# Optimization experiments

Hardware: AMD Instinct MI355X
Metric: run time of the kernel (lower is better)

The kernel has to match this reference:

```python
import jax, jax.numpy as jnp
import numpy as np
from jax.scipy.linalg import expm

B, S, D, E, K, NROT = 2, 2048, 1024, 8, 2, 3
EPS = 1e-5


def setup_inputs() -> dict:
    key = jax.random.key(0)
    ks = jax.random.split(key, 16)
    sc = 0.02
    x = jax.random.normal(ks[0], (B, S, D), jnp.float32)
    ln_gamma = 1.0 + sc * jax.random.normal(ks[1], (D,), jnp.float32)
    ln_beta = sc * jax.random.normal(ks[2], (D,), jnp.float32)
    abel_w = sc * jax.random.normal(ks[3], (D, D), jnp.float32)
    abel_b = sc * jax.random.normal(ks[4], (D,), jnp.float32)
    moe_gate_w = sc * jax.random.normal(ks[5], (D, E), jnp.float32)
    moe_gate_b = sc * jax.random.normal(ks[6], (E,), jnp.float32)
    ew1 = sc * jax.random.normal(ks[7], (E, D, 2 * D), jnp.float32)
    eb1 = sc * jax.random.normal(ks[8], (E, 2 * D), jnp.float32)
    ew2 = sc * jax.random.normal(ks[9], (E, 2 * D, D), jnp.float32)
    eb2 = sc * jax.random.normal(ks[10], (E, D), jnp.float32)
    g = sc * jax.random.normal(ks[11], (NROT, D, D), jnp.float32)
    gens = 0.5 * (g - jnp.swapaxes(g, -1, -2))  # skew-symmetric, as in reset_parameters
    gc_w = sc * jax.random.normal(ks[12], (2 * D, 1), jnp.float32)
    gc_b = sc * jax.random.normal(ks[13], (1,), jnp.float32)
    return dict(x=x, ln_gamma=ln_gamma, ln_beta=ln_beta, abel_w=abel_w, abel_b=abel_b,
                moe_gate_w=moe_gate_w, moe_gate_b=moe_gate_b, ew1=ew1, eb1=eb1,
                ew2=ew2, eb2=eb2, gens=gens, gc_w=gc_w, gc_b=gc_b)


def _gelu(x):
    return jax.nn.gelu(x, approximate=False)  # torch nn.GELU default = exact erf


def _forward(x, ln_gamma, ln_beta, abel_w, abel_b, moe_gate_w, moe_gate_b,
             ew1, eb1, ew2, eb2, gens, gc_w, gc_b):
    residual = x
    # LayerNorm
    mu = jnp.mean(x, axis=-1, keepdims=True)
    var = jnp.mean((x - mu) ** 2, axis=-1, keepdims=True)
    xn = (x - mu) * jax.lax.rsqrt(var + EPS) * ln_gamma + ln_beta
    # abel branch: Linear + GELU
    abel_out = _gelu(xn @ abel_w + abel_b)
    # MoE: dense all-experts compute, masked by top-k softmax weights
    logits = xn @ moe_gate_w + moe_gate_b                      # [B,S,E]
    topw, topi = jax.lax.top_k(logits, K)                      # [B,S,K]
    topw = jax.nn.softmax(topw, axis=-1)
    w_dense = jnp.sum(jax.nn.one_hot(topi, E, dtype=xn.dtype) * topw[..., None], axis=-2)  # [B,S,E]
    h = _gelu(jnp.einsum('bsd,edh->ebsh', xn, ew1) + eb1[:, None, None, :])  # [E,B,S,2D]
    eo = jnp.einsum('ebsh,ehd->ebsd', h, ew2) + eb2[:, None, None, :]        # [E,B,S,D]
    moe_out = jnp.einsum('ebsd,bse->bsd', eo, w_dense)
    # GeometricRotation: sequential matrix_exp rotations
    for i in range(NROT):
        moe_out = moe_out @ expm(gens[i])
    # gated residual mix
    combined = jnp.concatenate([abel_out, moe_out], axis=-1)
    gate = jax.nn.sigmoid(combined @ gc_w + gc_b)              # [B,S,1]
    mixed = abel_out * (1.0 - gate) + moe_out * gate
    return residual + mixed


def reference(x, ln_gamma, ln_beta, abel_w, abel_b, moe_gate_w, moe_gate_b,
              ew1, eb1, ew2, eb2, gens, gc_w, gc_b):
    return _forward(x, ln_gamma, ln_beta, abel_w, abel_b, moe_gate_w, moe_gate_b,
                    ew1, eb1, ew2, eb2, gens, gc_w, gc_b)
```

## Files before the change

kernel.cpp:

```cpp
#include <hip/hip_runtime.h>
#include <hip/hip_bf16.h>
#include <cstdint>
#include <cstddef>

#define DD   1024
#define DD2  2048
#define EE   8
#define NTOK 4096
#define CAPR 9216
#define MAXT 72

typedef __bf16 bf16_t;
typedef __bf16 bf16x8 __attribute__((ext_vector_type(8)));
typedef __bf16 bf16x4 __attribute__((ext_vector_type(4)));
typedef float  f32x4v __attribute__((ext_vector_type(4)));

__device__ __forceinline__ float gelu_f(float v){
  const float t = v*(0.7978845608028654f + 0.0356774081f*v*v);
  const float u = __expf(2.0f*t);
  return __fdividef(v*u, 1.0f + u);
}

__device__ __forceinline__ void gload_lds16(const void* g, void* l){
  __builtin_amdgcn_global_load_lds(
    (const __attribute__((address_space(1))) unsigned int*)(uintptr_t)g,
    (__attribute__((address_space(3))) unsigned int*)(uintptr_t)l,
    16, 0, 0);
}

enum { EPI_GELU_F32=0, EPI_GELU_BF16=1, EPI_BIAS_BF16=2, EPI_SCALE_BF16=3,
       EPI_ADDV_BF16=4, EPI_BF16=5, EPI_F32=6 };

template<int BM,int BN,int EPI,bool TAB>
__global__ __launch_bounds__(256)
void gemm_bt(const bf16_t* __restrict__ A, const bf16_t* __restrict__ Bt,
             const int N, const int K, const int gx, const int gy, const int gz,
             const long sAz, const long sBz, const long sOz,
             const int* __restrict__ tileE, const int* __restrict__ tileR,
             const int* __restrict__ ntp, const int* __restrict__ offp,
             const int* __restrict__ tokOf,
             const float* __restrict__ bias, const long sBias,
             const float alpha,
             const bf16_t* __restrict__ addv,
             float* __restrict__ outF, bf16_t* __restrict__ outB)
{
  constexpr int BK = 32;
  constexpr int WM = BM/2, WN = BN/2;
  constexpr int FM = WM/16, FN = WN/16;
  constexpr int IA = BM/64, IB = BN/64;
  constexpr int NLD = IA + IB;
  __shared__ alignas(16) bf16_t sA[3][BM*BK];
  __shared__ alignas(16) bf16_t sB[3][BN*BK];

  int bx, by, bz; long ro = 0;
  if constexpr (TAB) {
    const int nwg = gx * gy;
    const int q = nwg >> 3, r = nwg & 7;
    const int k = blockIdx.x & 7, i = blockIdx.x >> 3;
    if (i >= q + (k < r ? 1 : 0)) return;
    const int l = k * q + (k < r ? k : r) + i;
    const int ti = l / gx; bx = l - ti*gx;
    if (ti >= ntp[0]) return;
    bz = tileE[ti]; by = 0;
    ro = (long)offp[bz] + tileR[ti];
  } else {
    const int nwg = gx * gy * gz;
    const int q = nwg >> 3, r = nwg & 7;
    const int k = blockIdx.x & 7, i = blockIdx.x >> 3;
    if (i >= q + (k < r ? 1 : 0)) return;
    const int l = k * q + (k < r ? k : r) + i;
    bx = l % gx; const int t2 = l / gx; by = t2 % gy; bz = t2 / gy;
  }

  const int z = bz;
  const bf16_t* Bp = Bt + (size_t)z * sBz;
  float*  oF = outF;
  bf16_t* oB = outB;
  if constexpr (TAB) {
    oB += ro * (long)N;
  } else {
    A += (size_t)z * sAz;
    if (oF) oF += (size_t)z * sOz;
    if (oB) oB += (size_t)z * sOz;
  }
  const float*  bp = bias ? bias + (size_t)z * sBias : nullptr;
  const bf16_t* vp = addv ? addv + (size_t)z * sOz   : nullptr;

  const int tid = threadIdx.x;
  const int wid = tid >> 6, lid = tid & 63;
  const int wr = wid >> 1, wc = wid & 1;
  const int brow = by * BM, bcol = bx * BN;
  const int fr = lid & 15, fq = lid >> 4;
  const int rl = lid >> 2, qs = lid & 3;

  const char* aSrc[IA];
  const char* bSrc[IB];
  #pragma unroll
  for (int i = 0; i < IA; i++) {
    const int rloc = (wid*IA + i)*16 + rl;
    const int q = qs ^ ((rloc >> 1) & 3);
    const bf16_t* arow;
    if constexpr (TAB) {
      arow = tokOf ? (A + (size_t)tokOf[ro + rloc] * K)
                   : (A + (size_t)(ro + rloc) * K);
    } else {
      arow = A + (size_t)(brow + rloc) * K;
    }
    aSrc[i] = (const char*)arow + q*16;
  }
  #pragma unroll
  for (int i = 0; i < IB; i++) {
    const int rloc = (wid*IB + i)*16 + rl;
    const int q = qs ^ ((rloc >> 1) & 3);
    bSrc[i] = (const char*)(Bp + (size_t)(bcol + rloc) * K) + q*16;
  }

  f32x4v acc[FM][FN] = {};

  auto stage = [&](int buf, int kt) {
    #pragma unroll
    for (int i = 0; i < IA; i++)
      gload_lds16(aSrc[i] + (size_t)kt*2, (char*)sA[buf] + (wid*IA + i)*1024);
    #pragma unroll
    for (int i = 0; i < IB; i++)
      gload_lds16(bSrc[i] + (size_t)kt*2, (char*)sB[buf] + (wid*IB + i)*1024);
  };

  stage(0, 0);
  stage(1, BK);
  const int nk = K / BK;
  int b0 = 0, b1 = 1, b2 = 2;

  for (int t = 0; t < nk; ++t) {
    if (t < nk - 1) asm volatile("s_waitcnt vmcnt(%0)" :: "i"(NLD) : "memory");
    else            asm volatile("s_waitcnt vmcnt(0)" ::: "memory");
    __builtin_amdgcn_s_barrier();
    __builtin_amdgcn_sched_barrier(0);
    if (t + 2 < nk) stage(b2, (t + 2)*BK);

    bf16x8 af[FM], bb[FN];
    #pragma unroll
    for (int mi = 0; mi < FM; mi++) {
      const int r2 = wr*WM + mi*16 + fr;
      const int q = fq ^ ((r2 >> 1) & 3);
      af[mi] = *(const bf16x8*)((const char*)sA[b0] + r2*64 + q*16);
    }
    #pragma unroll
    for (int ni = 0; ni < FN; ni++) {
      const int r2 = wc*WN + ni*16 + fr;
      const int q = fq ^ ((r2 >> 1) & 3);
      bb[ni] = *(const bf16x8*)((const char*)sB[b0] + r2*64 + q*16);
    }
    #pragma unroll
    for (int mi = 0; mi < FM; mi++)
      #pragma unroll
      for (int ni = 0; ni < FN; ni++)
        acc[mi][ni] = __builtin_amdgcn_mfma_f32_16x16x32_bf16(
            af[mi], bb[ni], acc[mi][ni], 0, 0, 0);

    const int tb_ = b0; b0 = b1; b1 = b2; b2 = tb_;
  }

  #pragma unroll
  for (int mi = 0; mi < FM; mi++) {
    #pragma unroll
    for (int ni = 0; ni < FN; ni++) {
      const int rg0 = brow + wr*WM + mi*16 + fq*4;
      const int cg  = bcol + wc*WN + ni*16 + fr;
      #pragma unroll
      for (int i = 0; i < 4; i++) {
        const int rg = rg0 + i;
        float v = acc[mi][ni][i];
        if constexpr (EPI == EPI_GELU_F32) {
          v += bp[cg];
          oF[(size_t)rg*N + cg] = gelu_f(v);
        } else if constexpr (EPI == EPI_GELU_BF16) {
          v += bp[cg];
          oB[(size_t)rg*N + cg] = (bf16_t)gelu_f(v);
        } else if constexpr (EPI == EPI_BIAS_BF16) {
          v += bp[cg];
          oB[(size_t)rg*N + cg] = (bf16_t)v;
        } else if constexpr (EPI == EPI_SCALE_BF16) {
          oB[(size_t)rg*N + cg] = (bf16_t)(v * alpha);
        } else if constexpr (EPI == EPI_ADDV_BF16) {
          oB[(size_t)rg*N + cg] = (bf16_t)(v + (float)vp[(size_t)rg*N + cg]);
        } else if constexpr (EPI == EPI_BF16) {
          oB[(size_t)rg*N + cg] = (bf16_t)v;
        } else {
          oF[(size_t)rg*N + cg] = v;
        }
      }
    }
  }
}

__device__ __forceinline__ void tcvt_tile(const float* __restrict__ src,
                                          bf16_t* __restrict__ dst,
                                          int R, int C, int bx, int by,
                                          float (*t)[65]){
  const int c0 = bx*64, r0 = by*64;
  const int lx = threadIdx.x & 15, ly = threadIdx.x >> 4;
  #pragma unroll
  for (int i = 0; i < 4; i++) {
    const int row = r0 + ly + i*16;
    const float4 v = *(const float4*)(src + (size_t)row*C + c0 + lx*4);
    t[ly + i*16][lx*4+0] = v.x; t[ly + i*16][lx*4+1] = v.y;
    t[ly + i*16][lx*4+2] = v.z; t[ly + i*16][lx*4+3] = v.w;
  }
  __syncthreads();
  #pragma unroll
  for (int i = 0; i < 4; i++) {
    const int c = c0 + ly + i*16;
    bf16x4 o;
    #pragma unroll
    for (int j = 0; j < 4; j++) o[j] = (bf16_t)t[lx*4+j][ly + i*16];
    *(bf16x4*)(dst + (size_t)c*R + r0 + lx*4) = o;
  }
}

__global__ __launch_bounds__(256)
void prep_kernel(const float* __restrict__ abel_w, bf16_t* __restrict__ abel_wT,
                 const float* __restrict__ ew1, bf16_t* __restrict__ ew1T,
                 const float* __restrict__ ew2, bf16_t* __restrict__ ew2T,
                 const float* __restrict__ gens, bf16_t* __restrict__ Hn)
{
  __shared__ float t[64][65];
  const int bid = blockIdx.x;
  if (bid < 256) {
    tcvt_tile(abel_w, abel_wT, DD, DD, bid & 15, bid >> 4, t);
  } else if (bid < 4352) {
    const int i = bid - 256, z = i >> 9, r = i & 511;
    tcvt_tile(ew1 + (size_t)z*DD*DD2, ew1T + (size_t)z*DD2*DD, DD, DD2, r & 31, r >> 5, t);
  } else if (bid < 8448) {
    const int i = bid - 4352, z = i >> 9, r = i & 511;
    tcvt_tile(ew2 + (size_t)z*DD2*DD, ew2T + (size_t)z*DD*DD2, DD2, DD, r & 15, r >> 4, t);
  } else {
    const long i4 = ((long)(bid - 8448)*256 + threadIdx.x)*4;
    const float4 v = *(const float4*)(gens + i4);
    bf16x4 b; b[0]=(bf16_t)(-v.x); b[1]=(bf16_t)(-v.y);
    b[2]=(bf16_t)(-v.z); b[3]=(bf16_t)(-v.w);
    *(bf16x4*)(Hn + i4) = b;
  }
}

__global__ __launch_bounds__(256)
void tb16_kernel(const bf16_t* __restrict__ Ut, bf16_t* __restrict__ Tb){
  __shared__ bf16_t tile[32][33];
  const bf16_t* src = Ut + (size_t)(1 - blockIdx.z) * DD * DD;
  bf16_t*       dst = Tb + (size_t)blockIdx.z * DD * DD;
  const int c0 = blockIdx.x*32, r0 = blockIdx.y*32;
  #pragma unroll
  for (int i = 0; i < 4; i++)
    tile[threadIdx.y + i*8][threadIdx.x] = src[(size_t)(r0 + threadIdx.y + i*8)*DD + c0 + threadIdx.x];
  __syncthreads();
  #pragma unroll
  for (int i = 0; i < 4; i++)
    dst[(size_t)(c0 + threadIdx.y + i*8)*DD + r0 + threadIdx.x] = tile[threadIdx.x][threadIdx.y + i*8];
}

__global__ __launch_bounds__(256)
void vw_kernel(const bf16_t* __restrict__ Hn, const bf16_t* __restrict__ H2,
               bf16_t* __restrict__ Vb, bf16_t* __restrict__ Wtb){
  const long i0 = ((long)blockIdx.x*256 + threadIdx.x)*4;
  const long rc = i0 % (long)(DD*DD);
  const int r = (int)(rc / DD), c0 = (int)(rc % DD);
  const bf16x4 h  = *(const bf16x4*)(Hn + i0);
  const bf16x4 h2 = *(const bf16x4*)(H2 + i0);
  bf16x4 v, w;
  #pragma unroll
  for (int j = 0; j < 4; j++) {
    const float d  = (r == c0 + j) ? 1.0f : 0.0f;
    const float fh = (float)h[j], f2 = (float)h2[j];
    v[j] = (bf16_t)(d + fh + f2*0.5f);
    w[j] = (bf16_t)(d*(1.0f/6.0f) - fh*(1.0f/24.0f) + f2*(1.0f/120.0f));
  }
  *(bf16x4*)(Vb  + i0) = v;
  *(bf16x4*)(Wtb + i0) = w;
}

__global__ __launch_bounds__(256)
void ln_gate_kernel(const float* __restrict__ x, const float* __restrict__ gamma,
                    const float* __restrict__ beta, const float* __restrict__ gw,
                    const float* __restrict__ gb,
                    bf16_t* __restrict__ xnb, int2* __restrict__ ids,
                    float2* __restrict__ wts)
{
  const int t = blockIdx.x, tid = threadIdx.x, j0 = tid*4;
  const int wid = tid >> 6, lid = tid & 63;
  const float4 v = *(const float4*)(x + (size_t)t*DD + j0);
  float s  = v.x + v.y + v.z + v.w;
  float ss = v.x*v.x + v.y*v.y + v.z*v.z + v.w*v.w;
  #pragma unroll
  for (int off = 32; off; off >>= 1) { s += __shfl_down(s, off); ss += __shfl_down(ss, off); }
  __shared__ float redS[4], redQ[4], mv[2];
  if (lid == 0) { redS[wid] = s; redQ[wid] = ss; }
  __syncthreads();
  if (tid == 0) {
    const float S1 = redS[0]+redS[1]+redS[2]+redS[3];
    const float S2 = redQ[0]+redQ[1]+redQ[2]+redQ[3];
    const float mu  = S1 * (1.0f/DD);
    const float var = S2 * (1.0f/DD) - mu*mu;
    mv[0] = mu; mv[1] = rsqrtf(var + 1e-5f);
  }
  __syncthreads();
  const float mu = mv[0], rstd = mv[1];
  const float4 g = *(const float4*)(gamma + j0);
  const float4 b = *(const float4*)(beta  + j0);
  float xn[4];
  xn[0] = (v.x-mu)*rstd*g.x + b.x;
  xn[1] = (v.y-mu)*rstd*g.y + b.y;
  xn[2] = (v.z-mu)*rstd*g.z + b.z;
  xn[3] = (v.w-mu)*rstd*g.w + b.w;
  bf16x4 ov; ov[0]=(bf16_t)xn[0]; ov[1]=(bf16_t)xn[1]; ov[2]=(bf16_t)xn[2]; ov[3]=(bf16_t)xn[3];
  *(bf16x4*)(xnb + (size_t)t*DD + j0) = ov;

  float p[8] = {0,0,0,0,0,0,0,0};
  #pragma unroll
  for (int i = 0; i < 4; i++) {
    const float4 a0 = *(const float4*)(gw + (size_t)(j0+i)*EE);
    const float4 a1 = *(const float4*)(gw + (size_t)(j0+i)*EE + 4);
    const float xv = xn[i];
    p[0]+=xv*a0.x; p[1]+=xv*a0.y; p[2]+=xv*a0.z; p[3]+=xv*a0.w;
    p[4]+=xv*a1.x; p[5]+=xv*a1.y; p[6]+=xv*a1.z; p[7]+=xv*a1.w;
  }
  #pragma unroll
  for (int off = 32; off; off >>= 1) {
    #pragma unroll
    for (int e = 0; e < 8; e++) p[e] += __shfl_down(p[e], off);
  }
  __shared__ float pr[32];
  if (lid == 0) {
    #pragma unroll
    for (int e = 0; e < 8; e++) pr[wid*8 + e] = p[e];
  }
  __syncthreads();
  if (tid == 0) {
    float l[8];
    #pragma unroll
    for (int e = 0; e < 8; e++) l[e] = pr[e] + pr[8+e] + pr[16+e] + pr[24+e] + gb[e];
    int i1 = 0; float m1 = l[0];
    #pragma unroll
    for (int e = 1; e < 8; e++) if (l[e] > m1) { m1 = l[e]; i1 = e; }
    int i2 = 0; float m2 = -1e30f;
    #pragma unroll
    for (int e = 0; e < 8; e++) if (e != i1 && l[e] > m2) { m2 = l[e]; i2 = e; }
    const float wa = 1.0f/(1.0f + expf(m2 - m1));
    ids[t] = make_int2(i1, i2);
    wts[t] = make_float2(wa, 1.0f - wa);
  }
}

__global__ __launch_bounds__(256)
void route_kernel(const int2* __restrict__ ids, int* __restrict__ slotA,
                  int* __restrict__ slotB, int* __restrict__ cnt,
                  int* __restrict__ off, int* __restrict__ tileE,
                  int* __restrict__ tileR, int* __restrict__ ntp)
{
  const int tid = threadIdx.x;
  const int wid = tid >> 6, lid = tid & 63;
  __shared__ int wsum[EE][4];
  __shared__ int base[EE];
  if (tid < EE) base[tid] = 0;
  __syncthreads();
  const unsigned long long lt = (1ull << lid) - 1ull;
  for (int c0 = 0; c0 < NTOK; c0 += 256) {
    const int t = c0 + tid;
    const int2 id = ids[t];
    int pA = 0, pB = 0;
    #pragma unroll
    for (int e = 0; e < EE; e++) {
      const bool fA = (id.x == e), fB = (id.y == e);
      const unsigned long long mA = __ballot(fA);
      const unsigned long long mB = __ballot(fB);
      const int cA = __popcll(mA);
      if (lid == 0) wsum[e][wid] = cA + __popcll(mB);
      if (fA) pA = __popcll(mA & lt);
      if (fB) pB = cA + __popcll(mB & lt);
    }
    __syncthreads();
    int wbA = base[id.x], wbB = base[id.y];
    for (int w = 0; w < wid; w++) { wbA += wsum[id.x][w]; wbB += wsum[id.y][w]; }
    slotA[t] = wbA + pA;
    slotB[t] = wbB + pB;
    __syncthreads();
    if (tid < EE) base[tid] += wsum[tid][0]+wsum[tid][1]+wsum[tid][2]+wsum[tid][3];
    __syncthreads();
  }
  if (tid == 0) {
    int a = 0, nt = 0;
    for (int e = 0; e < EE; e++) {
      cnt[e] = base[e]; off[e] = a;
      for (int r2 = 0; r2 < base[e]; r2 += 128) { tileE[nt] = e; tileR[nt] = r2; nt++; }
      a += (base[e] + 127) & ~127;
    }
    ntp[0] = nt;
  }
}

__global__ __launch_bounds__(256)
void fill_tok_kernel(const int2* __restrict__ ids, const int* __restrict__ slotA,
                     const int* __restrict__ slotB, const int* __restrict__ off,
                     const int* __restrict__ cnt, int* __restrict__ tokOf){
  const int t = blockIdx.x*256 + threadIdx.x;
  const int2 id = ids[t];
  tokOf[off[id.x] + slotA[t]] = t;
  tokOf[off[id.y] + slotB[t]] = t;
  if (blockIdx.x == 0) {
    for (int e = 0; e < EE; e++) {
      const int c = cnt[e], o = off[e], al = (c + 127) & ~127;
      for (int p = c + threadIdx.x; p < al; p += 256) tokOf[o + p] = 0;
    }
  }
}

__global__ __launch_bounds__(256)
void combine_kernel(const bf16_t* __restrict__ Yg, const int2* __restrict__ ids,
                    const int* __restrict__ slotA, const int* __restrict__ slotB,
                    const int* __restrict__ off, const float2* __restrict__ wts,
                    bf16_t* __restrict__ Xa){
  const int t = blockIdx.x, j = threadIdx.x*4;
  const int2 id = ids[t];
  const float2 w = wts[t];
  const bf16x4 a = *(const bf16x4*)(Yg + (size_t)(off[id.x] + slotA[t])*DD + j);
  const bf16x4 b = *(const bf16x4*)(Yg + (size_t)(off[id.y] + slotB[t])*DD + j);
  bf16x4 o;
  #pragma unroll
  for (int i = 0; i < 4; i++) o[i] = (bf16_t)(w.x*(float)a[i] + w.y*(float)b[i]);
  *(bf16x4*)(Xa + (size_t)t*DD + j) = o;
}

__global__ __launch_bounds__(256)
void mix_kernel(const float* __restrict__ x, const bf16_t* __restrict__ abel,
                const float* __restrict__ rot, const float* __restrict__ gcw,
                const float* __restrict__ gcb, float* __restrict__ out)
{
  const int t = blockIdx.x, tid = threadIdx.x, j0 = tid*4;
  const int wid = tid >> 6, lid = tid & 63;
  const bf16x4 ab = *(const bf16x4*)(abel + (size_t)t*DD + j0);
  const float4 r  = *(const float4*)(rot  + (size_t)t*DD + j0);
  const float4 ga = *(const float4*)(gcw + j0);
  const float4 gr = *(const float4*)(gcw + DD + j0);
  const float a0 = (float)ab[0], a1 = (float)ab[1], a2 = (float)ab[2], a3 = (float)ab[3];
  float p = a0*ga.x + a1*ga.y + a2*ga.z + a3*ga.w
          + r.x*gr.x + r.y*gr.y + r.z*gr.z + r.w*gr.w;
  #pragma unroll
  for (int off = 32; off; off >>= 1) p += __shfl_down(p, off);
  __shared__ float red[4];
  __shared__ float gsh;
  if (lid == 0) red[wid] = p;
  __syncthreads();
  if (tid == 0) {
    const float P = red[0] + red[1] + red[2] + red[3] + gcb[0];
    gsh = 1.0f/(1.0f + expf(-P));
  }
  __syncthreads();
  const float gate = gsh, g1 = 1.0f - gate;
  const float4 xv = *(const float4*)(x + (size_t)t*DD + j0);
  float4 o;
  o.x = xv.x + a0*g1 + r.x*gate;
  o.y = xv.y + a1*g1 + r.y*gate;
  o.z = xv.z + a2*g1 + r.z*gate;
  o.w = xv.w + a3*g1 + r.w*gate;
  *(float4*)(out + (size_t)t*DD + j0) = o;
}

extern "C" void kernel_launch(void* const* d_in, const int* in_sizes, int n_in,
                              void* d_out, int out_size, void* d_ws, size_t ws_size,
                              hipStream_t stream)
{
  (void)in_sizes; (void)n_in; (void)out_size; (void)ws_size;
  const float* x      = (const float*)d_in[0];
  const float* ln_g   = (const float*)d_in[1];
  const float* ln_b   = (const float*)d_in[2];
  const float* abel_w = (const float*)d_in[3];
  const float* abel_b = (const float*)d_in[4];
  const float* gate_w = (const float*)d_in[5];
  const float* gate_b = (const float*)d_in[6];
  const float* ew1    = (const float*)d_in[7];
  const float* eb1    = (const float*)d_in[8];
  const float* ew2    = (const float*)d_in[9];
  const float* eb2    = (const float*)d_in[10];
  const float* gens   = (const float*)d_in[11];
  const float* gc_w   = (const float*)d_in[12];
  const float* gc_b   = (const float*)d_in[13];
  float* out = (float*)d_out;

  char* wsp = (char*)d_ws;
  auto alloc = [&](size_t bytes) -> char* {
    char* p = wsp; wsp += (bytes + 255) & ~(size_t)255; return p;
  };
  const size_t MB = 1u<<20;
  bf16_t* xnb   = (bf16_t*)alloc((size_t)NTOK*DD*2);
  int2*   ids   = (int2*)  alloc((size_t)NTOK*8);
  float2* wts   = (float2*)alloc((size_t)NTOK*8);
  int*    slotA = (int*)   alloc((size_t)NTOK*4);
  int*    slotB = (int*)   alloc((size_t)NTOK*4);
  int*    cnt   = (int*)   alloc(64);
  int*    off   = (int*)   alloc(64);
  int*    tileE = (int*)   alloc(MAXT*4);
  int*    tileR = (int*)   alloc(MAXT*4);
  int*    ntp   = (int*)   alloc(64);
  int*    tokOf = (int*)   alloc((size_t)CAPR*4);
  bf16_t* abel_wT = (bf16_t*)alloc((size_t)DD*DD*2);
  char*   UN      = alloc(64*MB);
  bf16_t* ew1T  = (bf16_t*)UN;
  bf16_t* ew2T  = (bf16_t*)(UN + 32*MB);
  bf16_t* Hn    = (bf16_t*)alloc((size_t)3*DD*DD*2);
  bf16_t* abelo = (bf16_t*)alloc((size_t)NTOK*DD*2);
  bf16_t* Yg    = (bf16_t*)alloc((size_t)CAPR*DD*2);
  bf16_t* Hg    = (bf16_t*)alloc((size_t)CAPR*DD2*2);
  bf16_t* Xa    = (bf16_t*)alloc((size_t)NTOK*DD*2);
  float*  rot   = (float*)Hg;
  bf16_t* H2  = (bf16_t*)(UN + 0*MB);
  bf16_t* H3  = (bf16_t*)(UN + 6*MB);
  bf16_t* Vb  = (bf16_t*)(UN + 12*MB);
  bf16_t* Wtb = (bf16_t*)(UN + 18*MB);
  bf16_t* Ut  = (bf16_t*)(UN + 24*MB);
  bf16_t* Tb  = (bf16_t*)(UN + 30*MB);
  bf16_t* Pb  = (bf16_t*)(UN + 34*MB);
  bf16_t* Rt  = (bf16_t*)(UN + 36*MB);
  const long D2 = (long)DD*DD;

  auto gflat = [](int gx, int gy, int gz) {
    const int nwg = gx*gy*gz; return 8 * ((nwg + 7) / 8);
  };

  prep_kernel<<<dim3(11520,1,1), 256, 0, stream>>>(abel_w, abel_wT, ew1, ew1T,
                                                   ew2, ew2T, gens, Hn);

  ln_gate_kernel<<<dim3(NTOK,1,1), 256, 0, stream>>>(x, ln_g, ln_b, gate_w, gate_b,
                                                     xnb, ids, wts);
  route_kernel<<<dim3(1,1,1), 256, 0, stream>>>(ids, slotA, slotB, cnt, off,
                                                tileE, tileR, ntp);
  fill_tok_kernel<<<dim3(NTOK/256,1,1), 256, 0, stream>>>(ids, slotA, slotB, off, cnt, tokOf);

  gemm_bt<128,128,EPI_GELU_BF16,true><<<dim3((DD2/128)*MAXT,1,1), 256, 0, stream>>>(
      xnb, ew1T, DD2, DD, DD2/128, MAXT, 1, 0, (long)DD2*DD, 0,
      tileE, tileR, ntp, off, tokOf, eb1, DD2, 1.0f, nullptr, nullptr, Hg);
  gemm_bt<128,128,EPI_BIAS_BF16,true><<<dim3((DD/128)*MAXT,1,1), 256, 0, stream>>>(
      Hg, ew2T, DD, DD2, DD/128, MAXT, 1, 0, (long)DD*DD2, 0,
      tileE, tileR, ntp, off, nullptr, eb2, DD, 1.0f, nullptr, nullptr, Yg);
  combine_kernel<<<dim3(NTOK,1,1), 256, 0, stream>>>(Yg, ids, slotA, slotB, off, wts, Xa);

  gemm_bt<128,128,EPI_GELU_BF16,false><<<dim3(gflat(8,32,1),1,1), 256, 0, stream>>>(
      xnb, abel_wT, DD, DD, 8, 32, 1, 0, 0, 0, nullptr, nullptr, nullptr, nullptr,
      nullptr, abel_b, 0, 1.0f, nullptr, nullptr, abelo);

  gemm_bt<64,64,EPI_SCALE_BF16,false><<<dim3(gflat(16,16,3),1,1), 256, 0, stream>>>(
      Hn, Hn, DD, DD, 16, 16, 3, D2, D2, D2, nullptr, nullptr, nullptr, nullptr,
      nullptr, nullptr, 0, -1.0f, nullptr, nullptr, H2);
  gemm_bt<64,64,EPI_SCALE_BF16,false><<<dim3(gflat(16,16,3),1,1), 256, 0, stream>>>(
      H2, Hn, DD, DD, 16, 16, 3, D2, D2, D2, nullptr, nullptr, nullptr, nullptr,
      nullptr, nullptr, 0, -1.0f, nullptr, nullptr, H3);
  vw_kernel<<<dim3(3*DD*DD/1024,1,1), 256, 0, stream>>>(Hn, H2, Vb, Wtb);
  gemm_bt<64,64,EPI_ADDV_BF16,false><<<dim3(gflat(16,16,3),1,1), 256, 0, stream>>>(
      H3, Wtb, DD, DD, 16, 16, 3, D2, D2, D2, nullptr, nullptr, nullptr, nullptr,
      nullptr, nullptr, 0, 1.0f, Vb, nullptr, Ut);
  tb16_kernel<<<dim3(32,32,2), dim3(32,8,1), 0, stream>>>(Ut, Tb);
  gemm_bt<64,64,EPI_BF16,false><<<dim3(gflat(16,16,1),1,1), 256, 0, stream>>>(
      Ut + 2*D2, Tb, DD, DD, 16, 16, 1, 0, 0, 0, nullptr, nullptr, nullptr, nullptr,
      nullptr, nullptr, 0, 1.0f, nullptr, nullptr, Pb);
  gemm_bt<64,64,EPI_BF16,false><<<dim3(gflat(16,16,1),1,1), 256, 0, stream>>>(
      Pb, Tb + D2, DD, DD, 16, 16, 1, 0, 0, 0, nullptr, nullptr, nullptr, nullptr,
      nullptr, nullptr, 0, 1.0f, nullptr, nullptr, Rt);
  gemm_bt<128,128,EPI_F32,false><<<dim3(gflat(8,32,1),1,1), 256, 0, stream>>>(
      Xa, Rt, DD, DD, 8, 32, 1, 0, 0, 0, nullptr, nullptr, nullptr, nullptr,
      nullptr, nullptr, 0, 1.0f, nullptr, rot, nullptr);

  mix_kernel<<<dim3(NTOK,1,1), 256, 0, stream>>>(x, abelo, rot, gc_w, gc_b, out);
}
```

Baseline: 329.1 us.

## Use 256-row 8-wave tiles for expert GEMM1 and batch prep transposes

```diff
diff --git a/kernel.cpp b/kernel.cpp
--- a/kernel.cpp
+++ b/kernel.cpp
@@ -7,8 +7,9 @@
 #define DD2  2048
 #define EE   8
 #define NTOK 4096
-#define CAPR 9216
-#define MAXT 72
+#define CAPR 10240
+#define MAXT1 72
+#define MAXT2 40
 
 typedef __bf16 bf16_t;
 typedef __bf16 bf16x8 __attribute__((ext_vector_type(8)));
@@ -31,8 +32,8 @@
 enum { EPI_GELU_F32=0, EPI_GELU_BF16=1, EPI_BIAS_BF16=2, EPI_SCALE_BF16=3,
        EPI_ADDV_BF16=4, EPI_BF16=5, EPI_F32=6 };
 
-template<int BM,int BN,int EPI,bool TAB>
-__global__ __launch_bounds__(256)
+template<int BM,int BN,int WAVES,int EPI,bool TAB>
+__global__ __launch_bounds__(WAVES*64)
 void gemm_bt(const bf16_t* __restrict__ A, const bf16_t* __restrict__ Bt,
              const int N, const int K, const int gx, const int gy, const int gz,
              const long sAz, const long sBz, const long sOz,
@@ -45,9 +46,10 @@
              float* __restrict__ outF, bf16_t* __restrict__ outB)
 {
   constexpr int BK = 32;
-  constexpr int WM = BM/2, WN = BN/2;
+  constexpr int WROWS = WAVES/2;
+  constexpr int WM = BM/WROWS, WN = BN/2;
   constexpr int FM = WM/16, FN = WN/16;
-  constexpr int IA = BM/64, IB = BN/64;
+  constexpr int IA = BM/(16*WAVES), IB = BN/(16*WAVES);
   constexpr int NLD = IA + IB;
   __shared__ alignas(16) bf16_t sA[3][BM*BK];
   __shared__ alignas(16) bf16_t sB[3][BN*BK];
@@ -194,28 +196,25 @@
   }
 }
 
-__device__ __forceinline__ void tcvt_tile(const float* __restrict__ src,
-                                          bf16_t* __restrict__ dst,
-                                          int R, int C, int bx, int by,
-                                          float (*t)[65]){
-  const int c0 = bx*64, r0 = by*64;
-  const int lx = threadIdx.x & 15, ly = threadIdx.x >> 4;
-  #pragma unroll
-  for (int i = 0; i < 4; i++) {
-    const int row = r0 + ly + i*16;
-    const float4 v = *(const float4*)(src + (size_t)row*C + c0 + lx*4);
-    t[ly + i*16][lx*4+0] = v.x; t[ly + i*16][lx*4+1] = v.y;
-    t[ly + i*16][lx*4+2] = v.z; t[ly + i*16][lx*4+3] = v.w;
-  }
-  __syncthreads();
-  #pragma unroll
-  for (int i = 0; i < 4; i++) {
-    const int c = c0 + ly + i*16;
-    bf16x4 o;
-    #pragma unroll
-    for (int j = 0; j < 4; j++) o[j] = (bf16_t)t[lx*4+j][ly + i*16];
-    *(bf16x4*)(dst + (size_t)c*R + r0 + lx*4) = o;
-  }
+struct TileRef { const float* src; bf16_t* dst; int R, C, bx, by; };
+
+__device__ __forceinline__ TileRef resolve_tile(
+    int ti, const float* abel_w, bf16_t* abel_wT,
+    const float* ew1, bf16_t* ew1T, const float* ew2, bf16_t* ew2T){
+  TileRef tr;
+  if (ti < 256) {
+    tr.src = abel_w; tr.dst = abel_wT; tr.R = DD; tr.C = DD;
+    tr.bx = ti & 15; tr.by = ti >> 4;
+  } else if (ti < 4352) {
+    const int i = ti - 256, z = i >> 9, r = i & 511;
+    tr.src = ew1 + (size_t)z*DD*DD2; tr.dst = ew1T + (size_t)z*DD2*DD;
+    tr.R = DD; tr.C = DD2; tr.bx = r & 31; tr.by = r >> 5;
+  } else {
+    const int i = ti - 4352, z = i >> 9, r = i & 511;
+    tr.src = ew2 + (size_t)z*DD2*DD; tr.dst = ew2T + (size_t)z*DD*DD2;
+    tr.R = DD2; tr.C = DD; tr.bx = r & 15; tr.by = r >> 4;
+  }
+  return tr;
 }
 
 __global__ __launch_bounds__(256)
@@ -224,22 +223,57 @@
                  const float* __restrict__ ew2, bf16_t* __restrict__ ew2T,
                  const float* __restrict__ gens, bf16_t* __restrict__ Hn)
 {
-  __shared__ float t[64][65];
   const int bid = blockIdx.x;
-  if (bid < 256) {
-    tcvt_tile(abel_w, abel_wT, DD, DD, bid & 15, bid >> 4, t);
-  } else if (bid < 4352) {
-    const int i = bid - 256, z = i >> 9, r = i & 511;
-    tcvt_tile(ew1 + (size_t)z*DD*DD2, ew1T + (size_t)z*DD2*DD, DD, DD2, r & 31, r >> 5, t);
-  } else if (bid < 8448) {
-    const int i = bid - 4352, z = i >> 9, r = i & 511;
-    tcvt_tile(ew2 + (size_t)z*DD2*DD, ew2T + (size_t)z*DD*DD2, DD2, DD, r & 15, r >> 4, t);
+  const int lx = threadIdx.x & 15, ly = threadIdx.x >> 4;
+  if (bid < 4224) {
+    __shared__ float t[64][65];
+    const TileRef t0 = resolve_tile(bid*2,     abel_w, abel_wT, ew1, ew1T, ew2, ew2T);
+    const TileRef t1 = resolve_tile(bid*2 + 1, abel_w, abel_wT, ew1, ew1T, ew2, ew2T);
+    float4 g0[4], g1[4];
+    #pragma unroll
+    for (int i = 0; i < 4; i++)
+      g0[i] = *(const float4*)(t0.src + (size_t)(t0.by*64 + ly + i*16)*t0.C + t0.bx*64 + lx*4);
+    #pragma unroll
+    for (int i = 0; i < 4; i++)
+      g1[i] = *(const float4*)(t1.src + (size_t)(t1.by*64 + ly + i*16)*t1.C + t1.bx*64 + lx*4);
+    #pragma unroll
+    for (int i = 0; i < 4; i++) {
+      t[ly + i*16][lx*4+0] = g0[i].x; t[ly + i*16][lx*4+1] = g0[i].y;
+      t[ly + i*16][lx*4+2] = g0[i].z; t[ly + i*16][lx*4+3] = g0[i].w;
+    }
+    __syncthreads();
+    #pragma unroll
+    for (int i = 0; i < 4; i++) {
+      const int c = t0.bx*64 + ly + i*16;
+      bf16x4 o;
+      #pragma unroll
+      for (int j = 0; j < 4; j++) o[j] = (bf16_t)t[lx*4+j][ly + i*16];
+      *(bf16x4*)(t0.dst + (size_t)c*t0.R + t0.by*64 + lx*4) = o;
+    }
+    __syncthreads();
+    #pragma unroll
+    for (int i = 0; i < 4; i++) {
+      t[ly + i*16][lx*4+0] = g1[i].x; t[ly + i*16][lx*4+1] = g1[i].y;
+      t[ly + i*16][lx*4+2] = g1[i].z; t[ly + i*16][lx*4+3] = g1[i].w;
+    }
+    __syncthreads();
+    #pragma unroll
+    for (int i = 0; i < 4; i++) {
+      const int c = t1.bx*64 + ly + i*16;
+      bf16x4 o;
+      #pragma unroll
+      for (int j = 0; j < 4; j++) o[j] = (bf16_t)t[lx*4+j][ly + i*16];
+      *(bf16x4*)(t1.dst + (size_t)c*t1.R + t1.by*64 + lx*4) = o;
+    }
   } else {
-    const long i4 = ((long)(bid - 8448)*256 + threadIdx.x)*4;
-    const float4 v = *(const float4*)(gens + i4);
-    bf16x4 b; b[0]=(bf16_t)(-v.x); b[1]=(bf16_t)(-v.y);
-    b[2]=(bf16_t)(-v.z); b[3]=(bf16_t)(-v.w);
-    *(bf16x4*)(Hn + i4) = b;
+    #pragma unroll
+    for (int it = 0; it < 4; it++) {
+      const long i4 = (((long)(bid - 4224)*4 + it)*256 + threadIdx.x)*4;
+      const float4 v = *(const float4*)(gens + i4);
+      bf16x4 b; b[0]=(bf16_t)(-v.x); b[1]=(bf16_t)(-v.y);
+      b[2]=(bf16_t)(-v.z); b[3]=(bf16_t)(-v.w);
+      *(bf16x4*)(Hn + i4) = b;
+    }
   }
 }
 
@@ -353,8 +387,9 @@
 __global__ __launch_bounds__(256)
 void route_kernel(const int2* __restrict__ ids, int* __restrict__ slotA,
                   int* __restrict__ slotB, int* __restrict__ cnt,
-                  int* __restrict__ off, int* __restrict__ tileE,
-                  int* __restrict__ tileR, int* __restrict__ ntp)
+                  int* __restrict__ off, int* __restrict__ tE1,
+                  int* __restrict__ tR1, int* __restrict__ tE2,
+                  int* __restrict__ tR2, int* __restrict__ ntp)
 {
   const int tid = threadIdx.x;
   const int wid = tid >> 6, lid = tid & 63;
@@ -387,13 +422,14 @@
     __syncthreads();
   }
   if (tid == 0) {
-    int a = 0, nt = 0;
+    int a = 0, n1 = 0, n2 = 0;
     for (int e = 0; e < EE; e++) {
       cnt[e] = base[e]; off[e] = a;
-      for (int r2 = 0; r2 < base[e]; r2 += 128) { tileE[nt] = e; tileR[nt] = r2; nt++; }
-      a += (base[e] + 127) & ~127;
-    }
-    ntp[0] = nt;
+      for (int r2 = 0; r2 < base[e]; r2 += 128) { tE1[n1] = e; tR1[n1] = r2; n1++; }
+      for (int r2 = 0; r2 < base[e]; r2 += 256) { tE2[n2] = e; tR2[n2] = r2; n2++; }
+      a += (base[e] + 255) & ~255;
+    }
+    ntp[0] = n1; ntp[1] = n2;
   }
 }
 
@@ -407,7 +443,7 @@
   tokOf[off[id.y] + slotB[t]] = t;
   if (blockIdx.x == 0) {
     for (int e = 0; e < EE; e++) {
-      const int c = cnt[e], o = off[e], al = (c + 127) & ~127;
+      const int c = cnt[e], o = off[e], al = (c + 255) & ~255;
       for (int p = c + threadIdx.x; p < al; p += 256) tokOf[o + p] = 0;
     }
   }
@@ -497,8 +533,10 @@
   int*    slotB = (int*)   alloc((size_t)NTOK*4);
   int*    cnt   = (int*)   alloc(64);
   int*    off   = (int*)   alloc(64);
-  int*    tileE = (int*)   alloc(MAXT*4);
-  int*    tileR = (int*)   alloc(MAXT*4);
+  int*    tE1   = (int*)   alloc(MAXT1*4);
+  int*    tR1   = (int*)   alloc(MAXT1*4);
+  int*    tE2   = (int*)   alloc(MAXT2*4);
+  int*    tR2   = (int*)   alloc(MAXT2*4);
   int*    ntp   = (int*)   alloc(64);
   int*    tokOf = (int*)   alloc((size_t)CAPR*4);
   bf16_t* abel_wT = (bf16_t*)alloc((size_t)DD*DD*2);
@@ -525,45 +563,45 @@
     const int nwg = gx*gy*gz; return 8 * ((nwg + 7) / 8);
   };
 
-  prep_kernel<<<dim3(11520,1,1), 256, 0, stream>>>(abel_w, abel_wT, ew1, ew1T,
-                                                   ew2, ew2T, gens, Hn);
+  prep_kernel<<<dim3(4992,1,1), 256, 0, stream>>>(abel_w, abel_wT, ew1, ew1T,
+                                                  ew2, ew2T, gens, Hn);
 
   ln_gate_kernel<<<dim3(NTOK,1,1), 256, 0, stream>>>(x, ln_g, ln_b, gate_w, gate_b,
                                                      xnb, ids, wts);
   route_kernel<<<dim3(1,1,1), 256, 0, stream>>>(ids, slotA, slotB, cnt, off,
-                                                tileE, tileR, ntp);
+                                                tE1, tR1, tE2, tR2, ntp);
   fill_tok_kernel<<<dim3(NTOK/256,1,1), 256, 0, stream>>>(ids, slotA, slotB, off, cnt, tokOf);
 
-  gemm_bt<128,128,EPI_GELU_BF16,true><<<dim3((DD2/128)*MAXT,1,1), 256, 0, stream>>>(
-      xnb, ew1T, DD2, DD, DD2/128, MAXT, 1, 0, (long)DD2*DD, 0,
-      tileE, tileR, ntp, off, tokOf, eb1, DD2, 1.0f, nullptr, nullptr, Hg);
-  gemm_bt<128,128,EPI_BIAS_BF16,true><<<dim3((DD/128)*MAXT,1,1), 256, 0, stream>>>(
-      Hg, ew2T, DD, DD2, DD/128, MAXT, 1, 0, (long)DD*DD2, 0,
-      tileE, tileR, ntp, off, nullptr, eb2, DD, 1.0f, nullptr, nullptr, Yg);
+  gemm_bt<256,128,8,EPI_GELU_BF16,true><<<dim3(gflat(DD2/128, MAXT2, 1),1,1), 512, 0, stream>>>(
+      xnb, ew1T, DD2, DD, DD2/128, MAXT2, 1, 0, (long)DD2*DD, 0,
+      tE2, tR2, ntp + 1, off, tokOf, eb1, DD2, 1.0f, nullptr, nullptr, Hg);
+  gemm_bt<128,128,4,EPI_BIAS_BF16,true><<<dim3(gflat(DD/128, MAXT1, 1),1,1), 256, 0, stream>>>(
+      Hg, ew2T, DD, DD2, DD/128, MAXT1, 1, 0, (long)DD*DD2, 0,
+      tE1, tR1, ntp, off, nullptr, eb2, DD, 1.0f, nullptr, nullptr, Yg);
   combine_kernel<<<dim3(NTOK,1,1), 256, 0, stream>>>(Yg, ids, slotA, slotB, off, wts, Xa);
 
-  gemm_bt<128,128,EPI_GELU_BF16,false><<<dim3(gflat(8,32,1),1,1), 256, 0, stream>>>(
+  gemm_bt<128,128,4,EPI_GELU_BF16,false><<<dim3(gflat(8,32,1),1,1), 256, 0, stream>>>(
       xnb, abel_wT, DD, DD, 8, 32, 1, 0, 0, 0, nullptr, nullptr, nullptr, nullptr,
       nullptr, abel_b, 0, 1.0f, nullptr, nullptr, abelo);
 
-  gemm_bt<64,64,EPI_SCALE_BF16,false><<<dim3(gflat(16,16,3),1,1), 256, 0, stream>>>(
+  gemm_bt<64,64,4,EPI_SCALE_BF16,false><<<dim3(gflat(16,16,3),1,1), 256, 0, stream>>>(
       Hn, Hn, DD, DD, 16, 16, 3, D2, D2, D2, nullptr, nullptr, nullptr, nullptr,
       nullptr, nullptr, 0, -1.0f, nullptr, nullptr, H2);
-  gemm_bt<64,64,EPI_SCALE_BF16,false><<<dim3(gflat(16,16,3),1,1), 256, 0, stream>>>(
+  gemm_bt<64,64,4,EPI_SCALE_BF16,false><<<dim3(gflat(16,16,3),1,1), 256, 0, stream>>>(
       H2, Hn, DD, DD, 16, 16, 3, D2, D2, D2, nullptr, nullptr, nullptr, nullptr,
       nullptr, nullptr, 0, -1.0f, nullptr, nullptr, H3);
   vw_kernel<<<dim3(3*DD*DD/1024,1,1), 256, 0, stream>>>(Hn, H2, Vb, Wtb);
-  gemm_bt<64,64,EPI_ADDV_BF16,false><<<dim3(gflat(16,16,3),1,1), 256, 0, stream>>>(
+  gemm_bt<64,64,4,EPI_ADDV_BF16,false><<<dim3(gflat(16,16,3),1,1), 256, 0, stream>>>(
       H3, Wtb, DD, DD, 16, 16, 3, D2, D2, D2, nullptr, nullptr, nullptr, nullptr,
       nullptr, nullptr, 0, 1.0f, Vb, nullptr, Ut);
   tb16_kernel<<<dim3(32,32,2), dim3(32,8,1), 0, stream>>>(Ut, Tb);
-  gemm_bt<64,64,EPI_BF16,false><<<dim3(gflat(16,16,1),1,1), 256, 0, stream>>>(
+  gemm_bt<64,64,4,EPI_BF16,false><<<dim3(gflat(16,16,1),1,1), 256, 0, stream>>>(
       Ut + 2*D2, Tb, DD, DD, 16, 16, 1, 0, 0, 0, nullptr, nullptr, nullptr, nullptr,
       nullptr, nullptr, 0, 1.0f, nullptr, nullptr, Pb);
-  gemm_bt<64,64,EPI_BF16,false><<<dim3(gflat(16,16,1),1,1), 256, 0, stream>>>(
+  gemm_bt<64,64,4,EPI_BF16,false><<<dim3(gflat(16,16,1),1,1), 256, 0, stream>>>(
       Pb, Tb + D2, DD, DD, 16, 16, 1, 0, 0, 0, nullptr, nullptr, nullptr, nullptr,
       nullptr, nullptr, 0, 1.0f, nullptr, nullptr, Rt);
-  gemm_bt<128,128,EPI_F32,false><<<dim3(gflat(8,32,1),1,1), 256, 0, stream>>>(
+  gemm_bt<128,128,4,EPI_F32,false><<<dim3(gflat(8,32,1),1,1), 256, 0, stream>>>(
       Xa, Rt, DD, DD, 8, 32, 1, 0, 0, 0, nullptr, nullptr, nullptr, nullptr,
       nullptr, nullptr, 0, 1.0f, nullptr, rot, nullptr);
 
```

Result: slower. 337.8 us (+2.6%).
